# Performance work log

Measured on AMD Instinct MI355X. Metric: run time of the kernel, lower is better.

## Reference

```python
import jax, jax.numpy as jnp
import numpy as np
import math

H = 256; L = 4; ATOM_DIM = 100; TDIM = 128; NF = 10
B = 128; NN = 32; GS = 8
N = B * NN; E = B * NN * NN
DIS = NF * 2 * 3
DIN_E = 2 * H + 6 + DIS + 3
TWO_PI = 2.0 * math.pi

# symmetric 3x3 basis for CrystalFamily.v2m (log-lattice parameterization)
_b = np.zeros((6, 3, 3), np.float32)
_b[0, 0, 0] = 1.; _b[1, 1, 1] = 1.; _b[2, 2, 2] = 1.
_b[3, 0, 1] = _b[3, 1, 0] = 1.; _b[4, 0, 2] = _b[4, 2, 0] = 1.; _b[5, 1, 2] = _b[5, 2, 1] = 1.
BASIS = jnp.asarray(_b)


def _fwd(t, atom_types, frac_coords, lattices, G, k_mean, k_std, k_mask, k_bias,
         emb_w, emb_b, latent_w, latent_b, edge_w1, edge_b1, edge_w2, edge_b2,
         node_w1, node_b1, node_w2, node_b2, coord_w, lattice_w,
         node2graph, inv_G_permutation, group_size):
    # --- gen_edges: fully connected per graph (row-major, self-loops incl.) ---
    i = jnp.arange(NN)
    src_l = jnp.repeat(i, NN); dst_l = jnp.tile(i, NN)
    off = (jnp.arange(B) * NN)[:, None]
    src = (off + src_l[None, :]).reshape(-1)   # [E]
    dst = (off + dst_l[None, :]).reshape(-1)   # [E]
    e2g = jnp.repeat(jnp.arange(B), NN * NN)   # [E]
    # logmap frac diff
    z = TWO_PI * (frac_coords[dst] - frac_coords[src])
    frac_diff = jnp.arctan2(jnp.sin(z), jnp.cos(z)) / TWO_PI  # [E,3]
    # --- compute_frac_lattice_features ---
    y = lattices * k_std + k_mean
    y = y * k_mask + k_bias
    S = jnp.einsum('bk,kij->bij', y, BASIS)                    # [B,3,3]
    Lm = jax.vmap(jax.scipy.linalg.expm)(S)                    # v2m
    ltl = jnp.einsum('bji,bjk->bik', Lm, Lm)                   # L^T L
    ltl_f = jnp.einsum('eij,ej->ei', ltl[e2g], frac_diff)
    l_f = ltl_f / (jnp.linalg.norm(ltl_f, axis=-1, keepdims=True) + 1e-6)  # [E,3]
    # --- sinusoidal distance embedding (detached in original) ---
    freqs = TWO_PI * jnp.arange(NF, dtype=jnp.float32)
    de = (frac_diff[..., None] * freqs).reshape(E, 3 * NF)
    dis = jax.lax.stop_gradient(jnp.concatenate([jnp.sin(de), jnp.cos(de)], axis=-1))  # [E,60]
    # --- node embedding + time ---
    h = atom_types @ emb_w.T + emb_b
    half = TDIM // 2
    tf = jnp.exp(-math.log(10000.0) * jnp.arange(half, dtype=jnp.float32) / half)
    ta = t[:, None] * tf[None]
    temb = jnp.concatenate([jnp.cos(ta), jnp.sin(ta)], axis=-1)  # [B,TDIM] (cos first)
    tpa = jnp.repeat(temb, NN, axis=0)                           # repeat_interleave(num_atoms)
    h = jnp.concatenate([h, tpa], axis=-1) @ latent_w.T + latent_b
    # --- message passing layers ---
    lat_e = lattices[e2g]  # [E,6]
    deg = jax.ops.segment_sum(jnp.ones((E,), jnp.float32), src, num_segments=N)
    inv_deg = 1.0 / jnp.maximum(deg, 1.0)
    for l in range(L):
        ein = jnp.concatenate([h[src], h[dst], lat_e, dis, l_f], axis=-1)  # [E,581]
        ef = jax.nn.silu(ein @ edge_w1[l].T + edge_b1[l])
        ef = jax.nn.silu(ef @ edge_w2[l].T + edge_b2[l])
        agg = jax.ops.segment_sum(ef, src, num_segments=N) * inv_deg[:, None]  # scatter-mean
        nf = jnp.concatenate([h, agg], axis=-1)
        nf = jax.nn.silu(nf @ node_w1[l].T + node_b1[l])
        nf = jax.nn.silu(nf @ node_w2[l].T + node_b2[l])
        h = h + nf  # residual
    # --- heads ---
    graph_feat = jax.ops.segment_sum(h, node2graph, num_segments=B) / NN  # mean pool
    coord = h @ coord_w.T  # [N,3]
    # equivariant split-and-average
    x = coord.reshape(B, NN, 3)
    x = jnp.repeat(x, group_size, axis=0)                                   # [B*g,NN,3]
    x = jnp.take_along_axis(x, inv_G_permutation[:, :, None], axis=1)
    x = jnp.concatenate([x, jnp.ones((B * group_size, NN, 1), x.dtype)], axis=-1)
    zc = jnp.einsum('bni,bji->bnj', x, G)[:, :, :3]
    out_x = zc.reshape(B, group_size, NN, 3).mean(axis=1).reshape(N, 3)
    lattice_out = graph_feat @ lattice_w.T
    return out_x, lattice_out


def setup_inputs() -> dict:
    key = jax.random.key(0)
    ks = jax.random.split(key, 40)
    w = lambda k, s: jax.random.normal(k, s, jnp.float32) * 0.02
    inp = {}
    inp['t'] = jax.random.uniform(ks[0], (B,))
    inp['atom_types'] = jax.random.normal(ks[1], (N, ATOM_DIM))
    inp['frac_coords'] = jax.random.uniform(ks[2], (N, 3))
    inp['lattices'] = jax.random.normal(ks[3], (B, 6)) * 0.1
    inp['G'] = jnp.eye(4)[None] + 0.1 * jax.random.normal(ks[4], (B * GS, 4, 4))
    inp['k_mean'] = jax.random.normal(ks[5], (6,)) * 0.1
    inp['k_std'] = jnp.ones((6,))
    inp['k_mask'] = jnp.ones((6,))
    inp['k_bias'] = jnp.zeros((6,))
    inp['emb_w'] = w(ks[6], (H, ATOM_DIM)); inp['emb_b'] = jnp.zeros((H,))
    inp['latent_w'] = w(ks[7], (H, H + TDIM)); inp['latent_b'] = jnp.zeros((H,))
    inp['edge_w1'] = w(ks[8], (L, H, DIN_E)); inp['edge_b1'] = jnp.zeros((L, H))
    inp['edge_w2'] = w(ks[9], (L, H, H)); inp['edge_b2'] = jnp.zeros((L, H))
    inp['node_w1'] = w(ks[10], (L, H, 2 * H)); inp['node_b1'] = jnp.zeros((L, H))
    inp['node_w2'] = w(ks[11], (L, H, H)); inp['node_b2'] = jnp.zeros((L, H))
    inp['coord_w'] = w(ks[12], (3, H))
    inp['lattice_w'] = w(ks[13], (6, H))
    inp['num_atoms'] = jnp.full((B,), NN, jnp.int32)
    inp['node2graph'] = jnp.repeat(jnp.arange(B, dtype=jnp.int32), NN)
    pk = jax.random.split(ks[14], B * GS)
    inp['inv_G_permutation'] = jax.vmap(lambda k: jax.random.permutation(k, NN))(pk).astype(jnp.int32)
    inp['group_size'] = GS
    inp['tensor_group_size'] = jnp.full((B,), GS, jnp.int32)
    return inp


def reference(t, atom_types, frac_coords, lattices, G, k_mean, k_std, k_mask, k_bias,
              emb_w, emb_b, latent_w, latent_b, edge_w1, edge_b1, edge_w2, edge_b2,
              node_w1, node_b1, node_w2, node_b2, coord_w, lattice_w,
              num_atoms, node2graph, inv_G_permutation, group_size, tensor_group_size):
    return _fwd(t, atom_types, frac_coords, lattices, G, k_mean, k_std, k_mask, k_bias,
                emb_w, emb_b, latent_w, latent_b, edge_w1, edge_b1, edge_w2, edge_b2,
                node_w1, node_b1, node_w2, node_b2, coord_w, lattice_w,
                node2graph, inv_G_permutation, group_size)
```

## Files before the change

kernel.cpp:

```cpp
#include <hip/hip_runtime.h>
#include <math.h>

namespace {
constexpr int kH = 256;
constexpr int kL = 4;
constexpr int kAtomDim = 100;
constexpr int kB = 128;
constexpr int kNN = 32;
constexpr int kGS = 8;
constexpr int kN = kB * kNN;
constexpr int kE = kB * kNN * kNN;
constexpr int kDinE = 581;
constexpr int kKF = 96;
constexpr float kTwoPi = 6.28318530717958647692f;

typedef __bf16 bf16x8 __attribute__((ext_vector_type(8)));
typedef float  f32x4  __attribute__((ext_vector_type(4)));

__device__ __forceinline__ float fsilu(float x) {
    return x * __builtin_amdgcn_rcpf(1.0f + __expf(-x));
}

__global__ void lattice_kernel(const float* __restrict__ lattices,
                               const float* __restrict__ k_mean,
                               const float* __restrict__ k_std,
                               const float* __restrict__ k_mask,
                               const float* __restrict__ k_bias,
                               float* __restrict__ ltl) {
    int b = threadIdx.x;
    if (b >= kB) return;
    double y[6];
    for (int k = 0; k < 6; ++k) {
        double v = (double)lattices[b * 6 + k] * (double)k_std[k] + (double)k_mean[k];
        y[k] = v * (double)k_mask[k] + (double)k_bias[k];
    }
    double A[9] = { y[0], y[3], y[4],
                    y[3], y[1], y[5],
                    y[4], y[5], y[2] };
    double nrm = 0.0;
    for (int i = 0; i < 3; ++i) {
        double r = fabs(A[i*3+0]) + fabs(A[i*3+1]) + fabs(A[i*3+2]);
        nrm = fmax(nrm, r);
    }
    int s = 0;
    while (nrm > 0.25 && s < 40) { nrm *= 0.5; s++; }
    double sc = 1.0;
    for (int i = 0; i < s; ++i) sc *= 0.5;
    for (int i = 0; i < 9; ++i) A[i] *= sc;
    double T[9]    = {1,0,0, 0,1,0, 0,0,1};
    double term[9] = {1,0,0, 0,1,0, 0,0,1};
    for (int it = 1; it <= 18; ++it) {
        double nt[9];
        double inv = 1.0 / (double)it;
        for (int i = 0; i < 3; ++i)
            for (int j = 0; j < 3; ++j) {
                double acc = 0.0;
                for (int k = 0; k < 3; ++k) acc += term[i*3+k] * A[k*3+j];
                nt[i*3+j] = acc * inv;
            }
        for (int i = 0; i < 9; ++i) { term[i] = nt[i]; T[i] += nt[i]; }
    }
    for (int q = 0; q < s; ++q) {
        double nt[9];
        for (int i = 0; i < 3; ++i)
            for (int j = 0; j < 3; ++j) {
                double acc = 0.0;
                for (int k = 0; k < 3; ++k) acc += T[i*3+k] * T[k*3+j];
                nt[i*3+j] = acc;
            }
        for (int i = 0; i < 9; ++i) T[i] = nt[i];
    }
    for (int i = 0; i < 3; ++i)
        for (int k = 0; k < 3; ++k) {
            double acc = 0.0;
            for (int j = 0; j < 3; ++j) acc += T[j*3+i] * T[j*3+k];
            ltl[b*9 + i*3 + k] = (float)acc;
        }
}

__global__ void feats_bf_kernel(const float* __restrict__ frac,
                                const float* __restrict__ lattices,
                                const float* __restrict__ ltl,
                                __bf16* __restrict__ out) {
    int e = blockIdx.x * blockDim.x + threadIdx.x;
    if (e >= kE) return;
    int g = e >> 10;
    int src = (g << 5) + ((e >> 5) & 31);
    int dst = (g << 5) + (e & 31);
    float d[3];
    #pragma unroll
    for (int c = 0; c < 3; ++c) {
        float z = kTwoPi * (frac[dst*3 + c] - frac[src*3 + c]);
        d[c] = atan2f(sinf(z), cosf(z)) * (1.0f / kTwoPi);
    }
    __attribute__((aligned(16))) __bf16 f[kKF];
    #pragma unroll
    for (int k = 0; k < 6; ++k) f[k] = (__bf16)lattices[g*6 + k];
    #pragma unroll
    for (int c = 0; c < 3; ++c)
        #pragma unroll
        for (int fr = 0; fr < 10; ++fr) {
            float v = d[c] * (kTwoPi * (float)fr);
            f[6  + c*10 + fr] = (__bf16)sinf(v);
            f[36 + c*10 + fr] = (__bf16)cosf(v);
        }
    float v0 = ltl[g*9+0]*d[0] + ltl[g*9+1]*d[1] + ltl[g*9+2]*d[2];
    float v1 = ltl[g*9+3]*d[0] + ltl[g*9+4]*d[1] + ltl[g*9+5]*d[2];
    float v2 = ltl[g*9+6]*d[0] + ltl[g*9+7]*d[1] + ltl[g*9+8]*d[2];
    float nr = sqrtf(v0*v0 + v1*v1 + v2*v2) + 1e-6f;
    f[66] = (__bf16)(v0/nr); f[67] = (__bf16)(v1/nr); f[68] = (__bf16)(v2/nr);
    #pragma unroll
    for (int k = 69; k < kKF; ++k) f[k] = (__bf16)0.0f;
    uint4* dstp = (uint4*)(out + (size_t)e * kKF);
    const uint4* srcp = (const uint4*)f;
    #pragma unroll
    for (int i = 0; i < kKF/8; ++i) dstp[i] = srcp[i];
}

__global__ void conv_f2b(const float* __restrict__ s, __bf16* __restrict__ d, int n) {
    int i = blockIdx.x * 256 + threadIdx.x;
    if (i < n) d[i] = (__bf16)s[i];
}
__global__ void conv_w1ab(const float* __restrict__ w1, __bf16* __restrict__ dst) {
    int i = blockIdx.x * 256 + threadIdx.x;
    int l = i >> 17;
    int rem = i & 131071;
    int r = rem >> 8;
    int k = rem & 255;
    float v = (r < 256) ? w1[((size_t)(l*256 + r))*kDinE + k]
                        : w1[((size_t)(l*256 + (r-256)))*kDinE + 256 + k];
    dst[i] = (__bf16)v;
}
__global__ void conv_w1c(const float* __restrict__ w1, __bf16* __restrict__ dst) {
    int i = blockIdx.x * 256 + threadIdx.x;
    int l = i / (256*kKF);
    int rem = i - l*256*kKF;
    int n = rem / kKF;
    int k = rem - n*kKF;
    float v = (k < 69) ? w1[((size_t)(l*256 + n))*kDinE + 512 + k] : 0.0f;
    dst[i] = (__bf16)v;
}
__global__ void conv_atom(const float* __restrict__ a, __bf16* __restrict__ d) {
    int i = blockIdx.x * 256 + threadIdx.x;
    int n = i >> 7, k = i & 127;
    d[i] = (__bf16)((k < kAtomDim) ? a[(size_t)n*kAtomDim + k] : 0.0f);
}
__global__ void conv_embw(const float* __restrict__ w, __bf16* __restrict__ d) {
    int i = blockIdx.x * 256 + threadIdx.x;
    int n = i >> 7, k = i & 127;
    d[i] = (__bf16)((k < kAtomDim) ? w[(size_t)n*kAtomDim + k] : 0.0f);
}
__global__ void temb_kernel(const float* __restrict__ t, __bf16* __restrict__ tecat) {
    int g = blockIdx.x;
    int tid = threadIdx.x;
    float tf = expf(-logf(10000.0f) * (float)(tid & 63) / 64.0f);
    float ta = t[g] * tf;
    float v = (tid < 64) ? cosf(ta) : sinf(ta);
    __bf16 bv = (__bf16)v;
    #pragma unroll
    for (int nl = 0; nl < kNN; ++nl)
        tecat[((size_t)(g*kNN + nl))*384 + 256 + tid] = bv;
}

template<int K, int EPI>
__global__ __launch_bounds__(256) void gemm64(
        const __bf16* __restrict__ A, int lda,
        const __bf16* __restrict__ W, int ldw,
        const float* __restrict__ bias,
        float* __restrict__ out0, float* __restrict__ out1,
        __bf16* __restrict__ outbf, int ldo,
        float* __restrict__ hmaster, __bf16* __restrict__ hcat) {
    constexpr int NC = K / 32;
    __shared__ __bf16 As[2][64*40];
    __shared__ __bf16 Bs[2][64*40];
    int tid = threadIdx.x;
    int lane = tid & 63;
    int wid = tid >> 6;
    int wm = wid >> 1, wn = wid & 1;
    int r16 = lane & 15, g4 = lane >> 4;
    int mbase = blockIdx.x * 64;
    int nbase = blockIdx.y * 64;
    int srow = tid >> 2, sseg = tid & 3;
    const __bf16* agp = A + (size_t)(mbase + srow)*lda + sseg*8;
    const __bf16* wgp = W + (size_t)(nbase + srow)*ldw + sseg*8;
    int woff = srow*40 + sseg*8;

    f32x4 acc[2][2] = {};
    uint4 ra, rb;
    ra = *(const uint4*)(agp);
    rb = *(const uint4*)(wgp);
    *(uint4*)&As[0][woff] = ra;
    *(uint4*)&Bs[0][woff] = rb;
    __syncthreads();
    for (int c = 0; c < NC; ++c) {
        int cur = c & 1;
        if (c + 1 < NC) {
            ra = *(const uint4*)(agp + (c+1)*32);
            rb = *(const uint4*)(wgp + (c+1)*32);
        }
        bf16x8 af[2], bfg[2];
        #pragma unroll
        for (int mt = 0; mt < 2; ++mt)
            af[mt] = *(const bf16x8*)&As[cur][(wm*32 + mt*16 + r16)*40 + g4*8];
        #pragma unroll
        for (int nt = 0; nt < 2; ++nt)
            bfg[nt] = *(const bf16x8*)&Bs[cur][(wn*32 + nt*16 + r16)*40 + g4*8];
        #pragma unroll
        for (int mt = 0; mt < 2; ++mt)
            #pragma unroll
            for (int nt = 0; nt < 2; ++nt)
                acc[mt][nt] = __builtin_amdgcn_mfma_f32_16x16x32_bf16(af[mt], bfg[nt], acc[mt][nt], 0, 0, 0);
        if (c + 1 < NC) {
            int nxt = cur ^ 1;
            *(uint4*)&As[nxt][woff] = ra;
            *(uint4*)&Bs[nxt][woff] = rb;
        }
        __syncthreads();
    }
    #pragma unroll
    for (int mt = 0; mt < 2; ++mt)
        #pragma unroll
        for (int nt = 0; nt < 2; ++nt) {
            int n = nbase + wn*32 + nt*16 + r16;
            #pragma unroll
            for (int r = 0; r < 4; ++r) {
                int m = mbase + wm*32 + mt*16 + g4*4 + r;
                float v = acc[mt][nt][r];
                if (EPI == 0) {
                    if (n < 256) out0[(size_t)m*256 + n] = v + bias[n];
                    else         out1[(size_t)m*256 + (n - 256)] = v;
                } else if (EPI == 2) {
                    outbf[(size_t)m*ldo + n] = (__bf16)fsilu(v + bias[n]);
                } else if (EPI == 3) {
                    float hv = hmaster[(size_t)m*256 + n] + fsilu(v + bias[n]);
                    hmaster[(size_t)m*256 + n] = hv;
                    hcat[(size_t)m*512 + n] = (__bf16)hv;
                } else if (EPI == 4) {
                    outbf[(size_t)m*ldo + n] = (__bf16)(v + bias[n]);
                } else if (EPI == 5) {
                    float hv = v + bias[n];
                    hmaster[(size_t)m*256 + n] = hv;
                    hcat[(size_t)m*512 + n] = (__bf16)hv;
                }
            }
        }
}

__global__ __launch_bounds__(256, 2) void fused_edge(
        const float* __restrict__ Sb, const float* __restrict__ Dq,
        const __bf16* __restrict__ fb, const __bf16* __restrict__ w1c,
        const __bf16* __restrict__ w2, const float* __restrict__ b2,
        __bf16* __restrict__ hcat) {
    __shared__ float  Ds[32][260];
    __shared__ float  Ss[4][260];
    __shared__ __bf16 W1s[32][112];
    __shared__ __bf16 W2s[256][40];
    __shared__ __bf16 As_[128][40];

    int tid = threadIdx.x;
    int lane = tid & 63;
    int w = tid >> 6;
    int r16 = lane & 15, g4 = lane >> 4;
    int ebase = blockIdx.x * 128;
    int graph = ebase >> 10;
    int s0 = ebase >> 5;

    bf16x8 fReg[2][3];
    #pragma unroll
    for (int half = 0; half < 2; ++half) {
        const __bf16* fp = fb + (size_t)(ebase + w*32 + half*16 + r16)*kKF + g4*8;
        #pragma unroll
        for (int kc = 0; kc < 3; ++kc)
            fReg[half][kc] = *(const bf16x8*)(fp + kc*32);
    }
    {
        int dl = tid >> 3, seg = tid & 7;
        const float4* src = (const float4*)(Dq + (size_t)(graph*32 + dl)*256 + seg*32);
        #pragma unroll
        for (int i = 0; i < 8; ++i)
            *(float4*)&Ds[dl][seg*32 + i*4] = src[i];
    }
    {
        int sl = tid >> 6, c4 = (tid & 63) * 4;
        *(float4*)&Ss[sl][c4] = *(const float4*)(Sb + (size_t)(s0 + sl)*256 + c4);
    }
    __syncthreads();

    f32x4 acc2[2][16] = {};
    for (int nc = 0; nc < 8; ++nc) {
        __syncthreads();
        if (tid < 128) {
            int row = tid >> 2, q = tid & 3;
            const uint4* src = (const uint4*)(w1c + (size_t)(nc*32 + row)*kKF + q*24);
            #pragma unroll
            for (int i = 0; i < 3; ++i)
                *(uint4*)&W1s[row][q*24 + i*8] = src[i];
        }
        #pragma unroll
        for (int p = 0; p < 4; ++p) {
            int row = (tid >> 2) + p*64, q = tid & 3;
            *(uint4*)&W2s[row][q*8] = *(const uint4*)(w2 + (size_t)row*256 + nc*32 + q*8);
        }
        __syncthreads();

        f32x4 acc1[2][2] = {};
        #pragma unroll
        for (int kc = 0; kc < 3; ++kc) {
            bf16x8 bg0 = *(const bf16x8*)&W1s[r16][kc*32 + g4*8];
            bf16x8 bg1 = *(const bf16x8*)&W1s[16 + r16][kc*32 + g4*8];
            acc1[0][0] = __builtin_amdgcn_mfma_f32_16x16x32_bf16(fReg[0][kc], bg0, acc1[0][0], 0, 0, 0);
            acc1[0][1] = __builtin_amdgcn_mfma_f32_16x16x32_bf16(fReg[0][kc], bg1, acc1[0][1], 0, 0, 0);
            acc1[1][0] = __builtin_amdgcn_mfma_f32_16x16x32_bf16(fReg[1][kc], bg0, acc1[1][0], 0, 0, 0);
            acc1[1][1] = __builtin_amdgcn_mfma_f32_16x16x32_bf16(fReg[1][kc], bg1, acc1[1][1], 0, 0, 0);
        }
        #pragma unroll
        for (int nt = 0; nt < 2; ++nt) {
            int lc = nt*16 + r16;
            int n  = nc*32 + lc;
            float sv = Ss[w][n];
            #pragma unroll
            for (int mt = 0; mt < 2; ++mt)
                #pragma unroll
                for (int r = 0; r < 4; ++r) {
                    int dl = mt*16 + g4*4 + r;
                    float v = acc1[mt][nt][r] + sv + Ds[dl][n];
                    As_[w*32 + dl][lc] = (__bf16)fsilu(v);
                }
        }
        __syncthreads();

        bf16x8 am0 = *(const bf16x8*)&As_[w*32 + r16][g4*8];
        bf16x8 am1 = *(const bf16x8*)&As_[w*32 + 16 + r16][g4*8];
        #pragma unroll
        for (int nt = 0; nt < 16; ++nt) {
            bf16x8 bv = *(const bf16x8*)&W2s[nt*16 + r16][g4*8];
            acc2[0][nt] = __builtin_amdgcn_mfma_f32_16x16x32_bf16(am0, bv, acc2[0][nt], 0, 0, 0);
            acc2[1][nt] = __builtin_amdgcn_mfma_f32_16x16x32_bf16(am1, bv, acc2[1][nt], 0, 0, 0);
        }
    }

    const float inv32 = 1.0f / 32.0f;
    #pragma unroll
    for (int nt = 0; nt < 16; ++nt) {
        int col = nt*16 + r16;
        float bb = b2[col];
        float p = 0.f;
        #pragma unroll
        for (int r = 0; r < 4; ++r)
            p += fsilu(acc2[0][nt][r] + bb) + fsilu(acc2[1][nt][r] + bb);
        p += __shfl_xor(p, 16);
        p += __shfl_xor(p, 32);
        if (lane < 16)
            hcat[(size_t)(s0 + w)*512 + 256 + col] = (__bf16)(p * inv32);
    }
}

__global__ void coord_equiv_kernel(const float* __restrict__ h,
                                   const float* __restrict__ coord_w,
                                   const float* __restrict__ G,
                                   const int* __restrict__ invp,
                                   float* __restrict__ out_x) {
    int b = blockIdx.x;
    int tid = threadIdx.x;
    __shared__ float cd[kNN][4];
    if (tid < kNN*3) {
        int nl = tid / 3, j = tid - nl*3;
        const float* hr = h + (size_t)(b*kNN + nl)*kH;
        const float* wr = coord_w + (size_t)j*kH;
        float acc = 0.f;
        #pragma unroll 4
        for (int k = 0; k < kH; ++k) acc += hr[k]*wr[k];
        cd[nl][j] = acc;
    }
    __syncthreads();
    if (tid < kNN*3) {
        int nl = tid / 3, j = tid - nl*3;
        float acc = 0.f;
        for (int g = 0; g < kGS; ++g) {
            int bg = b*kGS + g;
            int p = invp[bg*kNN + nl];
            const float* Gr = G + (size_t)bg*16 + j*4;
            acc += cd[p][0]*Gr[0] + cd[p][1]*Gr[1] + cd[p][2]*Gr[2] + Gr[3];
        }
        out_x[(size_t)(b*kNN + nl)*3 + j] = acc * (1.0f/kGS);
    }
}

__global__ void graphfeat_kernel(const float* __restrict__ h,
                                 const float* __restrict__ lattice_w,
                                 float* __restrict__ out_lat) {
    int g = blockIdx.x;
    int c = threadIdx.x;
    __shared__ float gf[kH];
    float s = 0.f;
    for (int nl = 0; nl < kNN; ++nl) s += h[(size_t)(g*kNN + nl)*kH + c];
    gf[c] = s * (1.0f/kNN);
    __syncthreads();
    if (c < 6) {
        const float* wr = lattice_w + (size_t)c*kH;
        float acc = 0.f;
        #pragma unroll 4
        for (int k = 0; k < kH; ++k) acc += gf[k]*wr[k];
        out_lat[g*6 + c] = acc;
    }
}

}

extern "C" void kernel_launch(void* const* d_in, const int* in_sizes, int n_in,
                              void* d_out, int out_size, void* d_ws, size_t ws_size,
                              hipStream_t stream) {
    (void)in_sizes; (void)n_in; (void)out_size; (void)ws_size;
    const float* t         = (const float*)d_in[0];
    const float* atom      = (const float*)d_in[1];
    const float* frac      = (const float*)d_in[2];
    const float* lattices  = (const float*)d_in[3];
    const float* G         = (const float*)d_in[4];
    const float* k_mean    = (const float*)d_in[5];
    const float* k_std     = (const float*)d_in[6];
    const float* k_mask    = (const float*)d_in[7];
    const float* k_bias    = (const float*)d_in[8];
    const float* emb_w     = (const float*)d_in[9];
    const float* emb_b     = (const float*)d_in[10];
    const float* latent_w  = (const float*)d_in[11];
    const float* latent_b  = (const float*)d_in[12];
    const float* edge_w1   = (const float*)d_in[13];
    const float* edge_b1   = (const float*)d_in[14];
    const float* edge_w2   = (const float*)d_in[15];
    const float* edge_b2   = (const float*)d_in[16];
    const float* node_w1   = (const float*)d_in[17];
    const float* node_b1   = (const float*)d_in[18];
    const float* node_w2   = (const float*)d_in[19];
    const float* node_b2   = (const float*)d_in[20];
    const float* coord_w   = (const float*)d_in[21];
    const float* lattice_w = (const float*)d_in[22];
    const int*   invp      = (const int*)d_in[25];

    float* out_x   = (float*)d_out;
    float* out_lat = (float*)d_out + kN*3;

    char* base = (char*)d_ws;
    size_t off = 0;
    auto carve = [&](size_t bytes) { char* p = base + off; off += bytes; return p; };
    float*  ltl    = (float*)carve(8192);
    float*  h      = (float*)carve(4194304);
    float*  Sbuf   = (float*)carve(4194304);
    float*  Dbuf   = (float*)carve(4194304);
    __bf16* hcat   = (__bf16*)carve(4194304);
    __bf16* t1     = (__bf16*)carve(2097152);
    __bf16* fb     = (__bf16*)carve(25165824);
    __bf16* w1ab   = (__bf16*)carve(1048576);
    __bf16* w1c    = (__bf16*)carve(262144);
    __bf16* w2b    = (__bf16*)carve(524288);
    __bf16* nw1b   = (__bf16*)carve(1048576);
    __bf16* nw2b   = (__bf16*)carve(524288);
    __bf16* at_bf  = (__bf16*)carve(1048576);
    __bf16* embwb  = (__bf16*)carve(65536);
    __bf16* latwb  = (__bf16*)carve(196608);
    __bf16* tecat  = (__bf16*)carve(3145728);

    lattice_kernel<<<1, 128, 0, stream>>>(lattices, k_mean, k_std, k_mask, k_bias, ltl);
    feats_bf_kernel<<<kE/256, 256, 0, stream>>>(frac, lattices, ltl, fb);
    conv_w1ab<<<(4*512*256)/256, 256, 0, stream>>>(edge_w1, w1ab);
    conv_w1c<<<(4*256*kKF)/256, 256, 0, stream>>>(edge_w1, w1c);
    conv_f2b<<<(4*256*256)/256, 256, 0, stream>>>(edge_w2, w2b, 4*256*256);
    conv_f2b<<<(4*256*512)/256, 256, 0, stream>>>(node_w1, nw1b, 4*256*512);
    conv_f2b<<<(4*256*256)/256, 256, 0, stream>>>(node_w2, nw2b, 4*256*256);
    conv_atom<<<(kN*128)/256, 256, 0, stream>>>(atom, at_bf);
    conv_embw<<<(256*128)/256, 256, 0, stream>>>(emb_w, embwb);
    conv_f2b<<<(256*384)/256, 256, 0, stream>>>(latent_w, latwb, 256*384);
    temb_kernel<<<kB, 128, 0, stream>>>(t, tecat);

    gemm64<128, 4><<<dim3(64, 4), 256, 0, stream>>>(
        at_bf, 128, embwb, 128, emb_b,
        nullptr, nullptr, tecat, 384, nullptr, nullptr);
    gemm64<384, 5><<<dim3(64, 4), 256, 0, stream>>>(
        tecat, 384, latwb, 384, latent_b,
        nullptr, nullptr, nullptr, 0, h, hcat);

    for (int l = 0; l < kL; ++l) {
        gemm64<256, 0><<<dim3(64, 8), 256, 0, stream>>>(
            hcat, 512, w1ab + (size_t)l*512*256, 256,
            edge_b1 + l*256, Sbuf, Dbuf, nullptr, 0, nullptr, nullptr);
        fused_edge<<<1024, 256, 0, stream>>>(
            Sbuf, Dbuf, fb, w1c + (size_t)l*256*kKF,
            w2b + (size_t)l*256*256, edge_b2 + l*256, hcat);
        gemm64<512, 2><<<dim3(64, 4), 256, 0, stream>>>(
            hcat, 512, nw1b + (size_t)l*256*512, 512,
            node_b1 + l*256, nullptr, nullptr, t1, 256, nullptr, nullptr);
        gemm64<256, 3><<<dim3(64, 4), 256, 0, stream>>>(
            t1, 256, nw2b + (size_t)l*256*256, 256,
            node_b2 + l*256, nullptr, nullptr, nullptr, 0, h, hcat);
    }
    coord_equiv_kernel<<<kB, 128, 0, stream>>>(h, coord_w, G, invp, out_x);
    graphfeat_kernel<<<kB, 256, 0, stream>>>(h, lattice_w, out_lat);
}
```

Baseline: 498.1 us.

## Cheapen edge feature trig, merge conversion kernels, prefetch weights in fused_edge

The edge feature kernel now wraps fractional differences with rint instead of atan2/sin/cos, and builds the harmonic sin/cos terms by angle-addition recurrence from a single sin/cos per axis. The eight weight and input conversion kernels are merged into one launch to cut launch overhead. In fused_edge, the next chunk's W1/W2 tiles are loaded into registers while the current chunk computes, hiding global load latency at the cost of extra registers. The recurrence can build up small rounding differences, but these are below bf16 precision.

```diff
diff --git a/kernel.cpp b/kernel.cpp
--- a/kernel.cpp
+++ b/kernel.cpp
@@ -90,20 +90,28 @@
     float d[3];
     #pragma unroll
     for (int c = 0; c < 3; ++c) {
-        float z = kTwoPi * (frac[dst*3 + c] - frac[src*3 + c]);
-        d[c] = atan2f(sinf(z), cosf(z)) * (1.0f / kTwoPi);
+        float delta = frac[dst*3 + c] - frac[src*3 + c];
+        d[c] = delta - rintf(delta);
     }
     __attribute__((aligned(16))) __bf16 f[kKF];
     #pragma unroll
     for (int k = 0; k < 6; ++k) f[k] = (__bf16)lattices[g*6 + k];
     #pragma unroll
-    for (int c = 0; c < 3; ++c)
-        #pragma unroll
-        for (int fr = 0; fr < 10; ++fr) {
-            float v = d[c] * (kTwoPi * (float)fr);
-            f[6  + c*10 + fr] = (__bf16)sinf(v);
-            f[36 + c*10 + fr] = (__bf16)cosf(v);
-        }
+    for (int c = 0; c < 3; ++c) {
+        float th = d[c] * kTwoPi;
+        float s1 = sinf(th), c1 = cosf(th);
+        float sk = 0.0f, ck = 1.0f;
+        f[6  + c*10] = (__bf16)0.0f;
+        f[36 + c*10] = (__bf16)1.0f;
+        #pragma unroll
+        for (int fr = 1; fr < 10; ++fr) {
+            float ns = sk*c1 + ck*s1;
+            float nc = ck*c1 - sk*s1;
+            sk = ns; ck = nc;
+            f[6  + c*10 + fr] = (__bf16)sk;
+            f[36 + c*10 + fr] = (__bf16)ck;
+        }
+    }
     float v0 = ltl[g*9+0]*d[0] + ltl[g*9+1]*d[1] + ltl[g*9+2]*d[2];
     float v1 = ltl[g*9+3]*d[0] + ltl[g*9+4]*d[1] + ltl[g*9+5]*d[2];
     float v2 = ltl[g*9+6]*d[0] + ltl[g*9+7]*d[1] + ltl[g*9+8]*d[2];
@@ -117,39 +125,60 @@
     for (int i = 0; i < kKF/8; ++i) dstp[i] = srcp[i];
 }
 
-__global__ void conv_f2b(const float* __restrict__ s, __bf16* __restrict__ d, int n) {
+constexpr int kW1abN = 4*512*256;
+constexpr int kW1cN  = 4*256*kKF;
+constexpr int kW2bN  = 4*256*256;
+constexpr int kNw1N  = 4*256*512;
+constexpr int kNw2N  = 4*256*256;
+constexpr int kAtN   = kN*128;
+constexpr int kEmbwN = 256*128;
+constexpr int kLatwN = 256*384;
+constexpr int kConvTotal = kW1abN + kW1cN + kW2bN + kNw1N + kNw2N + kAtN + kEmbwN + kLatwN;
+
+__global__ void conv_all(const float* __restrict__ edge_w1, const float* __restrict__ edge_w2,
+                         const float* __restrict__ node_w1, const float* __restrict__ node_w2,
+                         const float* __restrict__ atom, const float* __restrict__ emb_w,
+                         const float* __restrict__ latent_w,
+                         __bf16* __restrict__ w1ab, __bf16* __restrict__ w1c,
+                         __bf16* __restrict__ w2b, __bf16* __restrict__ nw1b,
+                         __bf16* __restrict__ nw2b, __bf16* __restrict__ at_bf,
+                         __bf16* __restrict__ embwb, __bf16* __restrict__ latwb) {
     int i = blockIdx.x * 256 + threadIdx.x;
-    if (i < n) d[i] = (__bf16)s[i];
-}
-__global__ void conv_w1ab(const float* __restrict__ w1, __bf16* __restrict__ dst) {
-    int i = blockIdx.x * 256 + threadIdx.x;
-    int l = i >> 17;
-    int rem = i & 131071;
-    int r = rem >> 8;
-    int k = rem & 255;
-    float v = (r < 256) ? w1[((size_t)(l*256 + r))*kDinE + k]
-                        : w1[((size_t)(l*256 + (r-256)))*kDinE + 256 + k];
-    dst[i] = (__bf16)v;
-}
-__global__ void conv_w1c(const float* __restrict__ w1, __bf16* __restrict__ dst) {
-    int i = blockIdx.x * 256 + threadIdx.x;
-    int l = i / (256*kKF);
-    int rem = i - l*256*kKF;
-    int n = rem / kKF;
-    int k = rem - n*kKF;
-    float v = (k < 69) ? w1[((size_t)(l*256 + n))*kDinE + 512 + k] : 0.0f;
-    dst[i] = (__bf16)v;
-}
-__global__ void conv_atom(const float* __restrict__ a, __bf16* __restrict__ d) {
-    int i = blockIdx.x * 256 + threadIdx.x;
-    int n = i >> 7, k = i & 127;
-    d[i] = (__bf16)((k < kAtomDim) ? a[(size_t)n*kAtomDim + k] : 0.0f);
-}
-__global__ void conv_embw(const float* __restrict__ w, __bf16* __restrict__ d) {
-    int i = blockIdx.x * 256 + threadIdx.x;
-    int n = i >> 7, k = i & 127;
-    d[i] = (__bf16)((k < kAtomDim) ? w[(size_t)n*kAtomDim + k] : 0.0f);
-}
+    if (i < kW1abN) {
+        int l = i >> 17, rem = i & 131071, r = rem >> 8, k = rem & 255;
+        float v = (r < 256) ? edge_w1[((size_t)(l*256 + r))*kDinE + k]
+                            : edge_w1[((size_t)(l*256 + (r-256)))*kDinE + 256 + k];
+        w1ab[i] = (__bf16)v;
+        return;
+    }
+    i -= kW1abN;
+    if (i < kW1cN) {
+        int l = i / (256*kKF), rem = i - l*256*kKF, n = rem / kKF, k = rem - n*kKF;
+        w1c[i] = (__bf16)((k < 69) ? edge_w1[((size_t)(l*256 + n))*kDinE + 512 + k] : 0.0f);
+        return;
+    }
+    i -= kW1cN;
+    if (i < kW2bN) { w2b[i] = (__bf16)edge_w2[i]; return; }
+    i -= kW2bN;
+    if (i < kNw1N) { nw1b[i] = (__bf16)node_w1[i]; return; }
+    i -= kNw1N;
+    if (i < kNw2N) { nw2b[i] = (__bf16)node_w2[i]; return; }
+    i -= kNw2N;
+    if (i < kAtN) {
+        int n = i >> 7, k = i & 127;
+        at_bf[i] = (__bf16)((k < kAtomDim) ? atom[(size_t)n*kAtomDim + k] : 0.0f);
+        return;
+    }
+    i -= kAtN;
+    if (i < kEmbwN) {
+        int n = i >> 7, k = i & 127;
+        embwb[i] = (__bf16)((k < kAtomDim) ? emb_w[(size_t)n*kAtomDim + k] : 0.0f);
+        return;
+    }
+    i -= kEmbwN;
+    if (i < kLatwN) { latwb[i] = (__bf16)latent_w[i]; return; }
+}
+
 __global__ void temb_kernel(const float* __restrict__ t, __bf16* __restrict__ tecat) {
     int g = blockIdx.x;
     int tid = threadIdx.x;
@@ -265,6 +294,10 @@
     int graph = ebase >> 10;
     int s0 = ebase >> 5;
 
+    int wrow = tid >> 2, wq = tid & 3;
+    uint4 w1r0, w1r1, w1r2;
+    uint4 w2r0, w2r1, w2r2, w2r3;
+
     bf16x8 fReg[2][3];
     #pragma unroll
     for (int half = 0; half < 2; ++half) {
@@ -283,6 +316,16 @@
     {
         int sl = tid >> 6, c4 = (tid & 63) * 4;
         *(float4*)&Ss[sl][c4] = *(const float4*)(Sb + (size_t)(s0 + sl)*256 + c4);
+    }
+    {
+        if (tid < 128) {
+            const uint4* src = (const uint4*)(w1c + (size_t)wrow*kKF + wq*24);
+            w1r0 = src[0]; w1r1 = src[1]; w1r2 = src[2];
+        }
+        w2r0 = *(const uint4*)(w2 + (size_t)(wrow      )*256 + wq*8);
+        w2r1 = *(const uint4*)(w2 + (size_t)(wrow +  64)*256 + wq*8);
+        w2r2 = *(const uint4*)(w2 + (size_t)(wrow + 128)*256 + wq*8);
+        w2r3 = *(const uint4*)(w2 + (size_t)(wrow + 192)*256 + wq*8);
     }
     __syncthreads();
 
@@ -290,16 +333,23 @@
     for (int nc = 0; nc < 8; ++nc) {
         __syncthreads();
         if (tid < 128) {
-            int row = tid >> 2, q = tid & 3;
-            const uint4* src = (const uint4*)(w1c + (size_t)(nc*32 + row)*kKF + q*24);
-            #pragma unroll
-            for (int i = 0; i < 3; ++i)
-                *(uint4*)&W1s[row][q*24 + i*8] = src[i];
-        }
-        #pragma unroll
-        for (int p = 0; p < 4; ++p) {
-            int row = (tid >> 2) + p*64, q = tid & 3;
-            *(uint4*)&W2s[row][q*8] = *(const uint4*)(w2 + (size_t)row*256 + nc*32 + q*8);
+            *(uint4*)&W1s[wrow][wq*24]      = w1r0;
+            *(uint4*)&W1s[wrow][wq*24 + 8]  = w1r1;
+            *(uint4*)&W1s[wrow][wq*24 + 16] = w1r2;
+        }
+        *(uint4*)&W2s[wrow      ][wq*8] = w2r0;
+        *(uint4*)&W2s[wrow +  64][wq*8] = w2r1;
+        *(uint4*)&W2s[wrow + 128][wq*8] = w2r2;
+        *(uint4*)&W2s[wrow + 192][wq*8] = w2r3;
+        if (nc + 1 < 8) {
+            if (tid < 128) {
+                const uint4* src = (const uint4*)(w1c + (size_t)((nc+1)*32 + wrow)*kKF + wq*24);
+                w1r0 = src[0]; w1r1 = src[1]; w1r2 = src[2];
+            }
+            w2r0 = *(const uint4*)(w2 + (size_t)(wrow      )*256 + (nc+1)*32 + wq*8);
+            w2r1 = *(const uint4*)(w2 + (size_t)(wrow +  64)*256 + (nc+1)*32 + wq*8);
+            w2r2 = *(const uint4*)(w2 + (size_t)(wrow + 128)*256 + (nc+1)*32 + wq*8);
+            w2r3 = *(const uint4*)(w2 + (size_t)(wrow + 192)*256 + (nc+1)*32 + wq*8);
         }
         __syncthreads();
 
@@ -461,14 +511,9 @@
 
     lattice_kernel<<<1, 128, 0, stream>>>(lattices, k_mean, k_std, k_mask, k_bias, ltl);
     feats_bf_kernel<<<kE/256, 256, 0, stream>>>(frac, lattices, ltl, fb);
-    conv_w1ab<<<(4*512*256)/256, 256, 0, stream>>>(edge_w1, w1ab);
-    conv_w1c<<<(4*256*kKF)/256, 256, 0, stream>>>(edge_w1, w1c);
-    conv_f2b<<<(4*256*256)/256, 256, 0, stream>>>(edge_w2, w2b, 4*256*256);
-    conv_f2b<<<(4*256*512)/256, 256, 0, stream>>>(node_w1, nw1b, 4*256*512);
-    conv_f2b<<<(4*256*256)/256, 256, 0, stream>>>(node_w2, nw2b, 4*256*256);
-    conv_atom<<<(kN*128)/256, 256, 0, stream>>>(atom, at_bf);
-    conv_embw<<<(256*128)/256, 256, 0, stream>>>(emb_w, embwb);
-    conv_f2b<<<(256*384)/256, 256, 0, stream>>>(latent_w, latwb, 256*384);
+    conv_all<<<(kConvTotal + 255)/256, 256, 0, stream>>>(
+        edge_w1, edge_w2, node_w1, node_w2, atom, emb_w, latent_w,
+        w1ab, w1c, w2b, nw1b, nw2b, at_bf, embwb, latwb);
     temb_kernel<<<kB, 128, 0, stream>>>(t, tecat);
 
     gemm64<128, 4><<<dim3(64, 4), 256, 0, stream>>>(
```

New measurement: 455.8 us. -8.5%, faster.
